# Optimization experiments

Measured on AMD Instinct MI355X. Metric: run time of the kernel, lower is better.

## Reference

```python
import jax, jax.numpy as jnp
import numpy as np

B, C, H, W = 2, 3, 256, 256
K_STEPS = 50
RHO = 0.5
SIGMA_INIT = float(0.5 / np.sqrt(2.0 * C))  # sigma_init == tau_init = 0.5/sqrt(C*2)


def nabla(x):
    # forward finite differences, zero at last row/col. x: [B,C,H,W] -> [B,C,2,H,W]
    dh = jnp.pad(x[:, :, 1:, :] - x[:, :, :-1, :], ((0, 0), (0, 0), (0, 1), (0, 0)))
    dw = jnp.pad(x[:, :, :, 1:] - x[:, :, :, :-1], ((0, 0), (0, 0), (0, 0), (0, 1)))
    return jnp.stack([dh, dw], axis=2)


def nablaT(u):
    # adjoint of nabla (negative divergence). u: [B,C,2,H,W] -> [B,C,H,W]
    v0, v1 = u[:, :, 0], u[:, :, 1]
    out = jnp.zeros(v0.shape, v0.dtype)
    out = out.at[:, :, 1:, :].add(v0[:, :, :-1, :]).at[:, :, :-1, :].add(-v0[:, :, :-1, :])
    out = out.at[:, :, :, 1:].add(v1[:, :, :, :-1]).at[:, :, :, :-1].add(-v1[:, :, :, :-1])
    return out


def l12_prox_conjugate(v, lamb):
    # Moreau: prox_{sigma*(lamb*f)*}(v) = v - sigma*prox_{(lamb/sigma) f}(v/sigma)
    # which for L12 reduces to projection onto the lamb-ball per group.
    # groups: l2 over axes (1,-2,-1) = (C,H,W), one group per (B, F).
    norm = jnp.sqrt(jnp.sum(v * v, axis=(1, 3, 4), keepdims=True))
    scale = lamb / jnp.maximum(norm, lamb)  # == min(1, lamb/norm), safe at 0
    return v * scale


def l2_prox(z, y, gamma):
    # argmin_u 0.5||u-z||^2 + gamma*0.5||u-y||^2  (A = identity)
    return (z + gamma * y) / (1.0 + gamma)


def setup_inputs() -> dict:
    key = jax.random.key(0)
    y = jax.random.normal(key, (B, C, H, W), dtype=jnp.float32)
    lambd = jnp.float32(-1.0)  # learnable scalar log-regularization weight
    return {"y": y, "lambd": lambd}


def reference(y, lambd):
    elambda = jnp.exp(lambd)
    # set_init: A_dagger = identity
    x0 = y
    xt0 = jnp.zeros_like(x0)
    u0 = nabla(x0)

    def step(carry, _):
        x, xt, u, sigma, tau = carry
        u_next = l12_prox_conjugate(u + sigma * nabla(xt), elambda)
        x_next = l2_prox(x - tau * nablaT(u_next), y, tau)
        chi = 1.0 / jnp.sqrt(1.0 + 2.0 * RHO * tau)
        tau_next = tau * chi
        sigma_next = sigma / chi
        xt_next = (1.0 + chi) * x_next - chi * x
        return (x_next, xt_next, u_next, sigma_next, tau_next), None

    init = (x0, xt0, u0, jnp.float32(SIGMA_INIT), jnp.float32(SIGMA_INIT))
    (x, xt, u, _, _), _ = jax.lax.scan(step, init, None, length=K_STEPS)
    return (x, xt, u)
```

## Files before the change

### kernel.cpp

```cpp
#include <hip/hip_runtime.h>
#include <math.h>

constexpr int Cc = 3, Hh = 256;
constexpr int NX = 393216;
constexpr int R = 8;
constexpr int NBLK = 192;
constexpr int KSTEPS = 50;
constexpr int ROWQ = 128;
constexpr int BROWS = 12;
constexpr int SLOTQ = NBLK * BROWS * ROWQ;
constexpr int PW = NBLK * 4;

using u64 = unsigned long long;
constexpr u64 SENT = 0x8000000080000000ull;

__device__ __forceinline__ float4 ld4(const float* p, int i) { return ((const float4*)p)[i]; }
__device__ __forceinline__ void st4(float* p, int i, float4 v) { ((float4*)p)[i] = v; }
__device__ __forceinline__ float4 mk4(float a, float b, float c, float d) { return make_float4(a, b, c, d); }
__device__ __forceinline__ u64 ldq(const u64* p) {
    return __hip_atomic_load(p, __ATOMIC_RELAXED, __HIP_MEMORY_SCOPE_AGENT);
}
__device__ __forceinline__ void stq(u64* p, u64 v) {
    __hip_atomic_store(p, v, __ATOMIC_RELAXED, __HIP_MEMORY_SCOPE_AGENT);
}
__device__ __forceinline__ void pub4(u64* w, float4 v) {
    union { float f[2]; u64 q; } a, b;
    a.f[0] = v.x; a.f[1] = v.y; b.f[0] = v.z; b.f[1] = v.w;
    stq(w, a.q); stq(w + 1, b.q);
}
__device__ __forceinline__ float4 unp(u64 lo, u64 hi) {
    union { u64 q; float f[2]; } a, b; a.q = lo; b.q = hi;
    return make_float4(a.f[0], a.f[1], b.f[0], b.f[1]);
}
__device__ __forceinline__ float4 col3(float4 P, float4 A, float4 B, float a, float b) {
    return mk4(fmaf(a, A.x, fmaf(b, B.x, P.x)), fmaf(a, A.y, fmaf(b, B.y, P.y)),
               fmaf(a, A.z, fmaf(b, B.z, P.z)), fmaf(a, A.w, fmaf(b, B.w, P.w)));
}
__device__ __forceinline__ float4 f4sub(float4 a, float4 b) {
    return mk4(a.x - b.x, a.y - b.y, a.z - b.z, a.w - b.w);
}
__device__ __forceinline__ float4 f4s(float4 a, float s) {
    return mk4(a.x * s, a.y * s, a.z * s, a.w * s);
}
__device__ __forceinline__ float4 f4fma(float s, float4 a, float4 b) {
    return mk4(fmaf(s, a.x, b.x), fmaf(s, a.y, b.y), fmaf(s, a.z, b.z), fmaf(s, a.w, b.w));
}
__device__ __forceinline__ float4 nth(float4 vm, bool up, float4 v0x, bool dn) {
    return mk4((up ? vm.x : 0.f) - (dn ? v0x.x : 0.f), (up ? vm.y : 0.f) - (dn ? v0x.y : 0.f),
               (up ? vm.z : 0.f) - (dn ? v0x.z : 0.f), (up ? vm.w : 0.f) - (dn ? v0x.w : 0.f));
}
__device__ __forceinline__ float4 ntw(float4 v1x, int c4) {
    float ul = __shfl_up(v1x.w, 1, 64);
    return mk4(((c4 > 0) ? ul : 0.f) - v1x.x, v1x.x - v1x.y, v1x.y - v1x.z,
               v1x.z - ((c4 < 63) ? v1x.w : 0.f));
}
__device__ __forceinline__ float4 gradw(float4 t, int c4) {
    float xn = __shfl_down(t.x, 1, 64);
    return mk4(t.y - t.x, t.z - t.y, t.w - t.z, (c4 < 63) ? (xn - t.w) : 0.f);
}
__device__ __forceinline__ void barld() {
    asm volatile("s_waitcnt lgkmcnt(0)" ::: "memory");
    __builtin_amdgcn_sched_barrier(0);
    __builtin_amdgcn_s_barrier();
    __builtin_amdgcn_sched_barrier(0);
}

__global__ void init_ws(u64* h0, u64* h1, u64* h2, u64* parts) {
    int i = blockIdx.x * 256 + threadIdx.x;
    if (i < SLOTQ) { h0[i] = SENT; h1[i] = SENT; h2[i] = SENT; }
    if (i < (KSTEPS + 1) * PW) parts[i] = SENT;
}

__global__ void __launch_bounds__(256, 1) cp_persist(
    const float* __restrict__ y, const float* __restrict__ lambd,
    float* __restrict__ xout, float* __restrict__ xtout, float* __restrict__ uout,
    u64* __restrict__ h0, u64* __restrict__ h1, u64* __restrict__ h2,
    u64* __restrict__ parts)
{
    __shared__ float sv0[8 * 256];
    __shared__ float sxtP[9 * 256];
    __shared__ float sxtA[9 * 256];
    __shared__ float sxtB[9 * 256];

    const int tid = threadIdx.x, blk = blockIdx.x;
    const int bc = blk >> 5, tile = blk & 31, r0 = tile * R;
    const int c4 = tid & 63, trow = tid >> 6;
    const int b = (bc >= Cc) ? 1 : 0;
    const float lamb = expf(lambd[0]);

    float4 yv[2], xcur[2], v0c[2], v1c[2];
    float4 xpP[2], xpA[2], xpB[2];
    float4 p0P[2], p0A[2], p0B[2], p1P[2], p1A[2], p1B[2];
    float4 yh = mk4(0, 0, 0, 0), vmtop = yh, v0h = yh, v1h = yh, xoh = yh;

    float tau = 0.20412414523193150818f;
    float sig = tau;
    float chi = 0.f, sigs = 0.f;
    float alpha = 0.f, beta = 0.f;

    auto slotp = [&](int r) -> u64* { return (r == 0) ? h0 : ((r == 1) ? h1 : h2); };

    auto wavesum2 = [&](float& a, float& bb) {
        #pragma unroll
        for (int m = 1; m < 64; m <<= 1) { a += __shfl_xor(a, m, 64); bb += __shfl_xor(bb, m, 64); }
    };

    auto pollscale = [&](int s) {
        const u64* pb = parts + (size_t)s * PW + b * (PW / 2) + c4 * 6;
        u64 q0, q1, q2, q3, q4, q5;
        for (;;) {
            q0 = ldq(pb); q1 = ldq(pb + 1); q2 = ldq(pb + 2);
            q3 = ldq(pb + 3); q4 = ldq(pb + 4); q5 = ldq(pb + 5);
            bool ok = (q0 != SENT) && (q1 != SENT) && (q2 != SENT) &&
                      (q3 != SENT) && (q4 != SENT) && (q5 != SENT);
            if (__all(ok)) break;
            __builtin_amdgcn_s_sleep(1);
        }
        asm volatile("" ::: "memory");
        float g0 = 0.f, g1 = 0.f;
        union { u64 q; float f[2]; } u_;
        u_.q = q0; g0 += u_.f[0]; g1 += u_.f[1];
        u_.q = q1; g0 += u_.f[0]; g1 += u_.f[1];
        u_.q = q2; g0 += u_.f[0]; g1 += u_.f[1];
        u_.q = q3; g0 += u_.f[0]; g1 += u_.f[1];
        u_.q = q4; g0 += u_.f[0]; g1 += u_.f[1];
        u_.q = q5; g0 += u_.f[0]; g1 += u_.f[1];
        wavesum2(g0, g1);
        alpha = lamb / fmaxf(sqrtf(g0), lamb);
        beta  = lamb / fmaxf(sqrtf(g1), lamb);
    };

    auto pubparts = [&](int s) {
        float pa0 = 0.f, pa1 = 0.f;
        #pragma unroll
        for (int k = 0; k < 2; ++k) {
            pa0 += v0c[k].x * v0c[k].x + v0c[k].y * v0c[k].y + v0c[k].z * v0c[k].z + v0c[k].w * v0c[k].w;
            pa1 += v1c[k].x * v1c[k].x + v1c[k].y * v1c[k].y + v1c[k].z * v1c[k].z + v1c[k].w * v1c[k].w;
        }
        wavesum2(pa0, pa1);
        if (c4 == 0) {
            union { float f[2]; u64 q; } pk; pk.f[0] = pa0; pk.f[1] = pa1;
            stq(parts + (size_t)s * PW + blk * 4 + trow, pk.q);
        }
    };

    auto expand = [&](u64* hb, bool pub) {
        const float inv = 1.f / (1.f + tau);
        const float tin = tau * inv;
        const float opc = 1.f + chi;
        float4 xtP[2], xtA[2], xtB[2];
        #pragma unroll
        for (int k = 0; k < 2; ++k) {
            const int rr = trow + 4 * k, gh = r0 + rr;
            float4 vm = (k == 0) ? ((trow > 0) ? ((float4*)(sv0 + (trow - 1) * 256))[c4] : vmtop)
                                 : ((float4*)(sv0 + (trow + 3) * 256))[c4];
            float4 NT0 = nth(vm, gh > 0, v0c[k], gh < Hh - 1);
            float4 NT1 = ntw(v1c[k], c4);
            float4 BASE = f4s(f4fma(tau, yv[k], xcur[k]), inv);
            float4 xA = f4s(NT0, -tin);
            float4 xB = f4s(NT1, -tin);
            xpP[k] = BASE; xpA[k] = xA; xpB[k] = xB;
            xtP[k] = f4fma(-chi, xcur[k], f4s(BASE, opc));
            xtA[k] = f4s(xA, opc);
            xtB[k] = f4s(xB, opc);
            if (rr >= 1) {
                ((float4*)(sxtP + rr * 256))[c4] = xtP[k];
                ((float4*)(sxtA + rr * 256))[c4] = xtA[k];
                ((float4*)(sxtB + rr * 256))[c4] = xtB[k];
            }
            if (pub && trow == 0 && k == 0) {
                u64* rbase = hb + ((size_t)blk * BROWS) * ROWQ;
                pub4(rbase +  9 * ROWQ + 2 * c4, BASE);
                pub4(rbase + 10 * ROWQ + 2 * c4, xA);
                pub4(rbase + 11 * ROWQ + 2 * c4, xB);
            }
        }
        if (trow == 0 && tile < 31) {
            float4 vmh = ((float4*)(sv0 + 7 * 256))[c4];
            float4 NT0h = nth(vmh, true, v0h, true);
            float4 NT1h = ntw(v1h, c4);
            float4 BASEh = f4s(f4fma(tau, yh, xoh), inv);
            float4 xAh = f4s(NT0h, -tin);
            float4 xBh = f4s(NT1h, -tin);
            ((float4*)(sxtP + 8 * 256))[c4] = f4fma(-chi, xoh, f4s(BASEh, opc));
            ((float4*)(sxtA + 8 * 256))[c4] = f4s(xAh, opc);
            ((float4*)(sxtB + 8 * 256))[c4] = f4s(xBh, opc);
        }
        barld();
        #pragma unroll
        for (int k = 0; k < 2; ++k) {
            const int rr = trow + 4 * k, gh = r0 + rr;
            float4 dhP = mk4(0, 0, 0, 0), dhA = dhP, dhB = dhP;
            if (gh < Hh - 1) {
                dhP = f4sub(((float4*)(sxtP + (rr + 1) * 256))[c4], xtP[k]);
                dhA = f4sub(((float4*)(sxtA + (rr + 1) * 256))[c4], xtA[k]);
                dhB = f4sub(((float4*)(sxtB + (rr + 1) * 256))[c4], xtB[k]);
            }
            float4 dwP = gradw(xtP[k], c4);
            float4 dwA = gradw(xtA[k], c4);
            float4 dwB = gradw(xtB[k], c4);
            p0P[k] = f4s(dhP, sigs);
            p0A[k] = f4fma(sigs, dhA, v0c[k]);
            p0B[k] = f4s(dhB, sigs);
            p1P[k] = f4s(dwP, sigs);
            p1A[k] = f4s(dwA, sigs);
            p1B[k] = f4fma(sigs, dwB, v1c[k]);
            if (pub) {
                u64* rbase = hb + ((size_t)blk * BROWS) * ROWQ;
                if (trow == 0 && k == 0) {
                    pub4(rbase + 3 * ROWQ + 2 * c4, p0P[0]);
                    pub4(rbase + 4 * ROWQ + 2 * c4, p0A[0]);
                    pub4(rbase + 5 * ROWQ + 2 * c4, p0B[0]);
                    pub4(rbase + 6 * ROWQ + 2 * c4, p1P[0]);
                    pub4(rbase + 7 * ROWQ + 2 * c4, p1A[0]);
                    pub4(rbase + 8 * ROWQ + 2 * c4, p1B[0]);
                }
                if (trow == 3 && k == 1) {
                    pub4(rbase + 0 * ROWQ + 2 * c4, p0P[1]);
                    pub4(rbase + 1 * ROWQ + 2 * c4, p0A[1]);
                    pub4(rbase + 2 * ROWQ + 2 * c4, p0B[1]);
                }
            }
        }
        barld();
    };

    {
        #pragma unroll
        for (int k = 0; k < 2; ++k) {
            const int rr = trow + 4 * k, gh = r0 + rr;
            const int j4 = bc * 16384 + gh * 64 + c4;
            yv[k] = ld4(y, j4);
            xcur[k] = yv[k];
            float4 dh = mk4(0, 0, 0, 0);
            if (gh < Hh - 1) dh = f4sub(ld4(y, j4 + 64), yv[k]);
            float4 dw = gradw(yv[k], c4);
            v0c[k] = dh; v1c[k] = dw;
            ((float4*)(sv0 + rr * 256))[c4] = dh;
        }
        if (trow == 0) {
            if (tile < 31) {
                const int j4h = bc * 16384 + (r0 + 8) * 64 + c4;
                yh = ld4(y, j4h);
                v0h = f4sub(ld4(y, j4h + 64), yh);
                v1h = gradw(yh, c4);
                xoh = yh;
            }
            if (tile > 0) {
                float4 ym = ld4(y, bc * 16384 + (r0 - 1) * 64 + c4);
                vmtop = f4sub(yv[0], ym);
            }
        }
        pubparts(1);
        chi = 1.f / sqrtf(1.f + tau);
        sigs = sig / chi;
        barld();
        expand(slotp(0), true);
        tau *= chi; sig = sigs;
    }

    for (int s = 1; s < KSTEPS; ++s) {
        pollscale(s);
        chi = 1.f / sqrtf(1.f + tau);
        sigs = sig / chi;

        #pragma unroll
        for (int k = 0; k < 2; ++k) {
            xcur[k] = col3(xpP[k], xpA[k], xpB[k], alpha, beta);
            v0c[k]  = col3(p0P[k], p0A[k], p0B[k], alpha, beta);
            v1c[k]  = col3(p1P[k], p1A[k], p1B[k], alpha, beta);
            ((float4*)(sv0 + (trow + 4 * k) * 256))[c4] = v0c[k];
        }
        u64* hbp = slotp((s - 1) % 3);
        if (trow == 0) {
            if (tile > 0) {
                const u64* ra = hbp + ((size_t)(blk - 1) * BROWS) * ROWQ + 2 * c4;
                u64 a0, a1, a2, a3, a4, a5;
                for (;;) {
                    a0 = ldq(ra);            a1 = ldq(ra + 1);
                    a2 = ldq(ra + ROWQ);     a3 = ldq(ra + ROWQ + 1);
                    a4 = ldq(ra + 2 * ROWQ); a5 = ldq(ra + 2 * ROWQ + 1);
                    if (__all((a0 != SENT) && (a1 != SENT) && (a2 != SENT) &&
                              (a3 != SENT) && (a4 != SENT) && (a5 != SENT))) break;
                    __builtin_amdgcn_s_sleep(1);
                }
                vmtop = col3(unp(a0, a1), unp(a2, a3), unp(a4, a5), alpha, beta);
            }
            if (tile < 31) {
                const u64* rb = hbp + ((size_t)(blk + 1) * BROWS) * ROWQ + 2 * c4;
                u64 b0, b1, b2, b3, b4, b5, b6, b7, b8, b9, b10, b11, b12, b13, b14, b15, b16, b17;
                for (;;) {
                    b0  = ldq(rb + 3 * ROWQ);  b1  = ldq(rb + 3 * ROWQ + 1);
                    b2  = ldq(rb + 4 * ROWQ);  b3  = ldq(rb + 4 * ROWQ + 1);
                    b4  = ldq(rb + 5 * ROWQ);  b5  = ldq(rb + 5 * ROWQ + 1);
                    b6  = ldq(rb + 6 * ROWQ);  b7  = ldq(rb + 6 * ROWQ + 1);
                    b8  = ldq(rb + 7 * ROWQ);  b9  = ldq(rb + 7 * ROWQ + 1);
                    b10 = ldq(rb + 8 * ROWQ);  b11 = ldq(rb + 8 * ROWQ + 1);
                    b12 = ldq(rb + 9 * ROWQ);  b13 = ldq(rb + 9 * ROWQ + 1);
                    b14 = ldq(rb + 10 * ROWQ); b15 = ldq(rb + 10 * ROWQ + 1);
                    b16 = ldq(rb + 11 * ROWQ); b17 = ldq(rb + 11 * ROWQ + 1);
                    bool ok = (b0 != SENT) && (b1 != SENT) && (b2 != SENT) && (b3 != SENT) &&
                              (b4 != SENT) && (b5 != SENT) && (b6 != SENT) && (b7 != SENT) &&
                              (b8 != SENT) && (b9 != SENT) && (b10 != SENT) && (b11 != SENT) &&
                              (b12 != SENT) && (b13 != SENT) && (b14 != SENT) && (b15 != SENT) &&
                              (b16 != SENT) && (b17 != SENT);
                    if (__all(ok)) break;
                    __builtin_amdgcn_s_sleep(1);
                }
                v0h = col3(unp(b0, b1),   unp(b2, b3),   unp(b4, b5),   alpha, beta);
                v1h = col3(unp(b6, b7),   unp(b8, b9),   unp(b10, b11), alpha, beta);
                xoh = col3(unp(b12, b13), unp(b14, b15), unp(b16, b17), alpha, beta);
            }
        }
        asm volatile("" ::: "memory");
        if (s <= 47) {
            u64* rb2 = slotp((s + 1) % 3) + ((size_t)blk * BROWS) * ROWQ;
            if (trow == 0) {
                #pragma unroll
                for (int r = 3; r < 12; ++r) {
                    stq(rb2 + r * ROWQ + 2 * c4, SENT);
                    stq(rb2 + r * ROWQ + 2 * c4 + 1, SENT);
                }
            } else if (trow == 3) {
                #pragma unroll
                for (int r = 0; r < 3; ++r) {
                    stq(rb2 + r * ROWQ + 2 * c4, SENT);
                    stq(rb2 + r * ROWQ + 2 * c4 + 1, SENT);
                }
            }
        }
        pubparts(s + 1);
        barld();
        expand(slotp(s % 3), s < KSTEPS - 1);
        tau *= chi; sig = sigs;
    }

    pollscale(KSTEPS);
    const float opc = 1.f + chi;
    #pragma unroll
    for (int k = 0; k < 2; ++k) {
        const int rr = trow + 4 * k, gh = r0 + rr;
        const int j4 = bc * 16384 + gh * 64 + c4;
        const int iv4 = bc * 32768 + gh * 64 + c4;
        float4 xf_ = col3(xpP[k], xpA[k], xpB[k], alpha, beta);
        float4 xtf = f4fma(-chi, xcur[k], f4s(xf_, opc));
        st4(xout, j4, xf_);
        st4(xtout, j4, xtf);
        st4(uout, iv4, f4s(v0c[k], alpha));
        st4(uout, iv4 + 16384, f4s(v1c[k], beta));
    }
}

extern "C" void kernel_launch(void* const* d_in, const int* in_sizes, int n_in,
                              void* d_out, int out_size, void* d_ws, size_t ws_size,
                              hipStream_t stream) {
    (void)in_sizes; (void)n_in; (void)out_size; (void)ws_size;
    const float* y     = (const float*)d_in[0];
    const float* lambd = (const float*)d_in[1];
    float* xout  = (float*)d_out;
    float* xtout = xout + NX;
    float* uout  = xout + 2 * NX;

    u64* h0 = (u64*)d_out;
    u64* h1 = h0 + SLOTQ;
    u64* h2 = (u64*)d_ws;
    u64* parts = h2 + SLOTQ;

    init_ws<<<SLOTQ / 256, 256, 0, stream>>>(h0, h1, h2, parts);
    cp_persist<<<NBLK, 256, 0, stream>>>(y, lambd, xout, xtout, uout, h0, h1, h2, parts);
}
```

Before: 211.4 us.

## Use 512 threads per block, one row per wave, and per-block norm partials

```diff
diff --git a/kernel.cpp b/kernel.cpp
--- a/kernel.cpp
+++ b/kernel.cpp
@@ -9,7 +9,6 @@
 constexpr int ROWQ = 128;
 constexpr int BROWS = 12;
 constexpr int SLOTQ = NBLK * BROWS * ROWQ;
-constexpr int PW = NBLK * 4;
 
 using u64 = unsigned long long;
 constexpr u64 SENT = 0x8000000080000000ull;
@@ -68,10 +67,10 @@
 __global__ void init_ws(u64* h0, u64* h1, u64* h2, u64* parts) {
     int i = blockIdx.x * 256 + threadIdx.x;
     if (i < SLOTQ) { h0[i] = SENT; h1[i] = SENT; h2[i] = SENT; }
-    if (i < (KSTEPS + 1) * PW) parts[i] = SENT;
-}
-
-__global__ void __launch_bounds__(256, 1) cp_persist(
+    if (i < (KSTEPS + 1) * NBLK) parts[i] = SENT;
+}
+
+__global__ void __launch_bounds__(512, 1) cp_persist(
     const float* __restrict__ y, const float* __restrict__ lambd,
     float* __restrict__ xout, float* __restrict__ xtout, float* __restrict__ uout,
     u64* __restrict__ h0, u64* __restrict__ h1, u64* __restrict__ h2,
@@ -81,16 +80,18 @@
     __shared__ float sxtP[9 * 256];
     __shared__ float sxtA[9 * 256];
     __shared__ float sxtB[9 * 256];
+    __shared__ float2 pw[8];
 
     const int tid = threadIdx.x, blk = blockIdx.x;
     const int bc = blk >> 5, tile = blk & 31, r0 = tile * R;
     const int c4 = tid & 63, trow = tid >> 6;
     const int b = (bc >= Cc) ? 1 : 0;
     const float lamb = expf(lambd[0]);
-
-    float4 yv[2], xcur[2], v0c[2], v1c[2];
-    float4 xpP[2], xpA[2], xpB[2];
-    float4 p0P[2], p0A[2], p0B[2], p1P[2], p1A[2], p1B[2];
+    const int gh = r0 + trow;
+    const int j4 = bc * 16384 + gh * 64 + c4;
+
+    float4 yv, xcur, v0c, v1c;
+    float4 xpP, xpA, xpB, p0P, p0A, p0B, p1P, p1A, p1B;
     float4 yh = mk4(0, 0, 0, 0), vmtop = yh, v0h = yh, v1h = yh, xoh = yh;
 
     float tau = 0.20412414523193150818f;
@@ -106,41 +107,39 @@
     };
 
     auto pollscale = [&](int s) {
-        const u64* pb = parts + (size_t)s * PW + b * (PW / 2) + c4 * 6;
-        u64 q0, q1, q2, q3, q4, q5;
+        const u64* pb = parts + (size_t)s * NBLK + b * 96;
+        const int i1 = 64 + (c4 & 31);
+        u64 q0, q1;
         for (;;) {
-            q0 = ldq(pb); q1 = ldq(pb + 1); q2 = ldq(pb + 2);
-            q3 = ldq(pb + 3); q4 = ldq(pb + 4); q5 = ldq(pb + 5);
-            bool ok = (q0 != SENT) && (q1 != SENT) && (q2 != SENT) &&
-                      (q3 != SENT) && (q4 != SENT) && (q5 != SENT);
-            if (__all(ok)) break;
+            q0 = ldq(pb + c4);
+            q1 = ldq(pb + i1);
+            if (__all((q0 != SENT) && (q1 != SENT))) break;
             __builtin_amdgcn_s_sleep(1);
         }
         asm volatile("" ::: "memory");
-        float g0 = 0.f, g1 = 0.f;
-        union { u64 q; float f[2]; } u_;
-        u_.q = q0; g0 += u_.f[0]; g1 += u_.f[1];
-        u_.q = q1; g0 += u_.f[0]; g1 += u_.f[1];
-        u_.q = q2; g0 += u_.f[0]; g1 += u_.f[1];
-        u_.q = q3; g0 += u_.f[0]; g1 += u_.f[1];
-        u_.q = q4; g0 += u_.f[0]; g1 += u_.f[1];
-        u_.q = q5; g0 += u_.f[0]; g1 += u_.f[1];
+        union { u64 q; float f[2]; } a;
+        a.q = q0;
+        float g0 = a.f[0], g1 = a.f[1];
+        a.q = q1;
+        if (c4 < 32) { g0 += a.f[0]; g1 += a.f[1]; }
         wavesum2(g0, g1);
         alpha = lamb / fmaxf(sqrtf(g0), lamb);
         beta  = lamb / fmaxf(sqrtf(g1), lamb);
     };
 
+    auto wavenorm = [&]() {
+        float pa0 = v0c.x*v0c.x + v0c.y*v0c.y + v0c.z*v0c.z + v0c.w*v0c.w;
+        float pa1 = v1c.x*v1c.x + v1c.y*v1c.y + v1c.z*v1c.z + v1c.w*v1c.w;
+        wavesum2(pa0, pa1);
+        if (c4 == 0) pw[trow] = make_float2(pa0, pa1);
+    };
     auto pubparts = [&](int s) {
-        float pa0 = 0.f, pa1 = 0.f;
-        #pragma unroll
-        for (int k = 0; k < 2; ++k) {
-            pa0 += v0c[k].x * v0c[k].x + v0c[k].y * v0c[k].y + v0c[k].z * v0c[k].z + v0c[k].w * v0c[k].w;
-            pa1 += v1c[k].x * v1c[k].x + v1c[k].y * v1c[k].y + v1c[k].z * v1c[k].z + v1c[k].w * v1c[k].w;
-        }
-        wavesum2(pa0, pa1);
-        if (c4 == 0) {
-            union { float f[2]; u64 q; } pk; pk.f[0] = pa0; pk.f[1] = pa1;
-            stq(parts + (size_t)s * PW + blk * 4 + trow, pk.q);
+        if (tid == 0) {
+            float q0 = 0.f, q1 = 0.f;
+            #pragma unroll
+            for (int w = 0; w < 8; ++w) { q0 += pw[w].x; q1 += pw[w].y; }
+            union { float f[2]; u64 q; } pk; pk.f[0] = q0; pk.f[1] = q1;
+            stq(parts + (size_t)s * NBLK + blk, pk.q);
         }
     };
 
@@ -148,27 +147,24 @@
         const float inv = 1.f / (1.f + tau);
         const float tin = tau * inv;
         const float opc = 1.f + chi;
-        float4 xtP[2], xtA[2], xtB[2];
-        #pragma unroll
-        for (int k = 0; k < 2; ++k) {
-            const int rr = trow + 4 * k, gh = r0 + rr;
-            float4 vm = (k == 0) ? ((trow > 0) ? ((float4*)(sv0 + (trow - 1) * 256))[c4] : vmtop)
-                                 : ((float4*)(sv0 + (trow + 3) * 256))[c4];
-            float4 NT0 = nth(vm, gh > 0, v0c[k], gh < Hh - 1);
-            float4 NT1 = ntw(v1c[k], c4);
-            float4 BASE = f4s(f4fma(tau, yv[k], xcur[k]), inv);
+        float4 xtP, xtA, xtB;
+        {
+            float4 vm = (trow > 0) ? ((float4*)(sv0 + (trow - 1) * 256))[c4] : vmtop;
+            float4 NT0 = nth(vm, gh > 0, v0c, gh < Hh - 1);
+            float4 NT1 = ntw(v1c, c4);
+            float4 BASE = f4s(f4fma(tau, yv, xcur), inv);
             float4 xA = f4s(NT0, -tin);
             float4 xB = f4s(NT1, -tin);
-            xpP[k] = BASE; xpA[k] = xA; xpB[k] = xB;
-            xtP[k] = f4fma(-chi, xcur[k], f4s(BASE, opc));
-            xtA[k] = f4s(xA, opc);
-            xtB[k] = f4s(xB, opc);
-            if (rr >= 1) {
-                ((float4*)(sxtP + rr * 256))[c4] = xtP[k];
-                ((float4*)(sxtA + rr * 256))[c4] = xtA[k];
-                ((float4*)(sxtB + rr * 256))[c4] = xtB[k];
-            }
-            if (pub && trow == 0 && k == 0) {
+            xpP = BASE; xpA = xA; xpB = xB;
+            xtP = f4fma(-chi, xcur, f4s(BASE, opc));
+            xtA = f4s(xA, opc);
+            xtB = f4s(xB, opc);
+            if (trow >= 1) {
+                ((float4*)(sxtP + trow * 256))[c4] = xtP;
+                ((float4*)(sxtA + trow * 256))[c4] = xtA;
+                ((float4*)(sxtB + trow * 256))[c4] = xtB;
+            }
+            if (pub && trow == 0) {
                 u64* rbase = hb + ((size_t)blk * BROWS) * ROWQ;
                 pub4(rbase +  9 * ROWQ + 2 * c4, BASE);
                 pub4(rbase + 10 * ROWQ + 2 * c4, xA);
@@ -187,38 +183,36 @@
             ((float4*)(sxtB + 8 * 256))[c4] = f4s(xBh, opc);
         }
         barld();
-        #pragma unroll
-        for (int k = 0; k < 2; ++k) {
-            const int rr = trow + 4 * k, gh = r0 + rr;
+        {
             float4 dhP = mk4(0, 0, 0, 0), dhA = dhP, dhB = dhP;
             if (gh < Hh - 1) {
-                dhP = f4sub(((float4*)(sxtP + (rr + 1) * 256))[c4], xtP[k]);
-                dhA = f4sub(((float4*)(sxtA + (rr + 1) * 256))[c4], xtA[k]);
-                dhB = f4sub(((float4*)(sxtB + (rr + 1) * 256))[c4], xtB[k]);
-            }
-            float4 dwP = gradw(xtP[k], c4);
-            float4 dwA = gradw(xtA[k], c4);
-            float4 dwB = gradw(xtB[k], c4);
-            p0P[k] = f4s(dhP, sigs);
-            p0A[k] = f4fma(sigs, dhA, v0c[k]);
-            p0B[k] = f4s(dhB, sigs);
-            p1P[k] = f4s(dwP, sigs);
-            p1A[k] = f4s(dwA, sigs);
-            p1B[k] = f4fma(sigs, dwB, v1c[k]);
+                dhP = f4sub(((float4*)(sxtP + (trow + 1) * 256))[c4], xtP);
+                dhA = f4sub(((float4*)(sxtA + (trow + 1) * 256))[c4], xtA);
+                dhB = f4sub(((float4*)(sxtB + (trow + 1) * 256))[c4], xtB);
+            }
+            float4 dwP = gradw(xtP, c4);
+            float4 dwA = gradw(xtA, c4);
+            float4 dwB = gradw(xtB, c4);
+            p0P = f4s(dhP, sigs);
+            p0A = f4fma(sigs, dhA, v0c);
+            p0B = f4s(dhB, sigs);
+            p1P = f4s(dwP, sigs);
+            p1A = f4s(dwA, sigs);
+            p1B = f4fma(sigs, dwB, v1c);
             if (pub) {
                 u64* rbase = hb + ((size_t)blk * BROWS) * ROWQ;
-                if (trow == 0 && k == 0) {
-                    pub4(rbase + 3 * ROWQ + 2 * c4, p0P[0]);
-                    pub4(rbase + 4 * ROWQ + 2 * c4, p0A[0]);
-                    pub4(rbase + 5 * ROWQ + 2 * c4, p0B[0]);
-                    pub4(rbase + 6 * ROWQ + 2 * c4, p1P[0]);
-                    pub4(rbase + 7 * ROWQ + 2 * c4, p1A[0]);
-                    pub4(rbase + 8 * ROWQ + 2 * c4, p1B[0]);
-                }
-                if (trow == 3 && k == 1) {
-                    pub4(rbase + 0 * ROWQ + 2 * c4, p0P[1]);
-                    pub4(rbase + 1 * ROWQ + 2 * c4, p0A[1]);
-                    pub4(rbase + 2 * ROWQ + 2 * c4, p0B[1]);
+                if (trow == 0) {
+                    pub4(rbase + 3 * ROWQ + 2 * c4, p0P);
+                    pub4(rbase + 4 * ROWQ + 2 * c4, p0A);
+                    pub4(rbase + 5 * ROWQ + 2 * c4, p0B);
+                    pub4(rbase + 6 * ROWQ + 2 * c4, p1P);
+                    pub4(rbase + 7 * ROWQ + 2 * c4, p1A);
+                    pub4(rbase + 8 * ROWQ + 2 * c4, p1B);
+                }
+                if (trow == 7) {
+                    pub4(rbase + 0 * ROWQ + 2 * c4, p0P);
+                    pub4(rbase + 1 * ROWQ + 2 * c4, p0A);
+                    pub4(rbase + 2 * ROWQ + 2 * c4, p0B);
                 }
             }
         }
@@ -226,18 +220,13 @@
     };
 
     {
-        #pragma unroll
-        for (int k = 0; k < 2; ++k) {
-            const int rr = trow + 4 * k, gh = r0 + rr;
-            const int j4 = bc * 16384 + gh * 64 + c4;
-            yv[k] = ld4(y, j4);
-            xcur[k] = yv[k];
-            float4 dh = mk4(0, 0, 0, 0);
-            if (gh < Hh - 1) dh = f4sub(ld4(y, j4 + 64), yv[k]);
-            float4 dw = gradw(yv[k], c4);
-            v0c[k] = dh; v1c[k] = dw;
-            ((float4*)(sv0 + rr * 256))[c4] = dh;
-        }
+        yv = ld4(y, j4);
+        xcur = yv;
+        float4 dh = mk4(0, 0, 0, 0);
+        if (gh < Hh - 1) dh = f4sub(ld4(y, j4 + 64), yv);
+        v0c = dh;
+        v1c = gradw(yv, c4);
+        ((float4*)(sv0 + trow * 256))[c4] = v0c;
         if (trow == 0) {
             if (tile < 31) {
                 const int j4h = bc * 16384 + (r0 + 8) * 64 + c4;
@@ -248,13 +237,14 @@
             }
             if (tile > 0) {
                 float4 ym = ld4(y, bc * 16384 + (r0 - 1) * 64 + c4);
-                vmtop = f4sub(yv[0], ym);
-            }
-        }
+                vmtop = f4sub(yv, ym);
+            }
+        }
+        wavenorm();
+        barld();
         pubparts(1);
         chi = 1.f / sqrtf(1.f + tau);
         sigs = sig / chi;
-        barld();
         expand(slotp(0), true);
         tau *= chi; sig = sigs;
     }
@@ -264,13 +254,11 @@
         chi = 1.f / sqrtf(1.f + tau);
         sigs = sig / chi;
 
-        #pragma unroll
-        for (int k = 0; k < 2; ++k) {
-            xcur[k] = col3(xpP[k], xpA[k], xpB[k], alpha, beta);
-            v0c[k]  = col3(p0P[k], p0A[k], p0B[k], alpha, beta);
-            v1c[k]  = col3(p1P[k], p1A[k], p1B[k], alpha, beta);
-            ((float4*)(sv0 + (trow + 4 * k) * 256))[c4] = v0c[k];
-        }
+        xcur = col3(xpP, xpA, xpB, alpha, beta);
+        v0c  = col3(p0P, p0A, p0B, alpha, beta);
+        v1c  = col3(p1P, p1A, p1B, alpha, beta);
+        ((float4*)(sv0 + trow * 256))[c4] = v0c;
+
         u64* hbp = slotp((s - 1) % 3);
         if (trow == 0) {
             if (tile > 0) {
@@ -313,6 +301,7 @@
             }
         }
         asm volatile("" ::: "memory");
+
         if (s <= 47) {
             u64* rb2 = slotp((s + 1) % 3) + ((size_t)blk * BROWS) * ROWQ;
             if (trow == 0) {
@@ -321,7 +310,7 @@
                     stq(rb2 + r * ROWQ + 2 * c4, SENT);
                     stq(rb2 + r * ROWQ + 2 * c4 + 1, SENT);
                 }
-            } else if (trow == 3) {
+            } else if (trow == 7) {
                 #pragma unroll
                 for (int r = 0; r < 3; ++r) {
                     stq(rb2 + r * ROWQ + 2 * c4, SENT);
@@ -329,26 +318,22 @@
                 }
             }
         }
+        wavenorm();
+        barld();
         pubparts(s + 1);
-        barld();
         expand(slotp(s % 3), s < KSTEPS - 1);
         tau *= chi; sig = sigs;
     }
 
     pollscale(KSTEPS);
     const float opc = 1.f + chi;
-    #pragma unroll
-    for (int k = 0; k < 2; ++k) {
-        const int rr = trow + 4 * k, gh = r0 + rr;
-        const int j4 = bc * 16384 + gh * 64 + c4;
-        const int iv4 = bc * 32768 + gh * 64 + c4;
-        float4 xf_ = col3(xpP[k], xpA[k], xpB[k], alpha, beta);
-        float4 xtf = f4fma(-chi, xcur[k], f4s(xf_, opc));
-        st4(xout, j4, xf_);
-        st4(xtout, j4, xtf);
-        st4(uout, iv4, f4s(v0c[k], alpha));
-        st4(uout, iv4 + 16384, f4s(v1c[k], beta));
-    }
+    const int iv4 = bc * 32768 + gh * 64 + c4;
+    float4 xf_ = col3(xpP, xpA, xpB, alpha, beta);
+    float4 xtf = f4fma(-chi, xcur, f4s(xf_, opc));
+    st4(xout, j4, xf_);
+    st4(xtout, j4, xtf);
+    st4(uout, iv4, f4s(v0c, alpha));
+    st4(uout, iv4 + 16384, f4s(v1c, beta));
 }
 
 extern "C" void kernel_launch(void* const* d_in, const int* in_sizes, int n_in,
@@ -367,5 +352,5 @@
     u64* parts = h2 + SLOTQ;
 
     init_ws<<<SLOTQ / 256, 256, 0, stream>>>(h0, h1, h2, parts);
-    cp_persist<<<NBLK, 256, 0, stream>>>(y, lambd, xout, xtout, uout, h0, h1, h2, parts);
-}
+    cp_persist<<<NBLK, 512, 0, stream>>>(y, lambd, xout, xtout, uout, h0, h1, h2, parts);
+}
```

Measured after the change: 208.5 us. No clear change (-1.4%).
